# Optimization experiments

Measured on AMD Instinct MI355X. Metric: run time of the kernel, lower is better.

Reference implementation:

```python
import jax, jax.numpy as jnp
import numpy as np

LN_EPS = 1e-6
KERNEL_EPS = 1e-3  # fast_attention generalized kernel_epsilon


def layer_norm(x, scale, bias):
    mu = jnp.mean(x, axis=-1, keepdims=True)
    var = jnp.mean(jnp.square(x - mu), axis=-1, keepdims=True)
    return (x - mu) * jax.lax.rsqrt(var + LN_EPS) * scale + bias


def sinusoidal_pos_emb(seq_len, dim):
    pos = jnp.arange(seq_len, dtype=jnp.float32)[:, None]
    div = jnp.exp(jnp.arange(0, dim, 2, dtype=jnp.float32) * (-np.log(10000.0) / dim))
    pe = jnp.zeros((seq_len, dim), dtype=jnp.float32)
    pe = pe.at[:, 0::2].set(jnp.sin(pos * div)).at[:, 1::2].set(jnp.cos(pos * div))
    return pe


def favor_generalized_attention(x, mask, wq, wk, wv, wo):
    # x: [B,S,E], mask: [B,S,1] (1 for real tokens), wq/wk/wv: [E,H,D], wo: [H,D,E]
    q = jnp.einsum('bse,ehd->bshd', x, wq)
    k = jnp.einsum('bse,ehd->bshd', x, wk)
    v = jnp.einsum('bse,ehd->bshd', x, wv)
    # deterministic generalized features: phi(x) = relu(x) + eps
    phi_q = jax.nn.relu(q) + KERNEL_EPS
    phi_k = (jax.nn.relu(k) + KERNEL_EPS) * mask[..., None]  # zero padded keys
    # bidirectional linear attention: O(S * H * D^2)
    kv = jnp.einsum('bshm,bshd->bhmd', phi_k, v)      # [B,H,D,D]
    z = jnp.sum(phi_k, axis=1)                        # [B,H,D]
    num = jnp.einsum('bshm,bhmd->bshd', phi_q, kv)    # [B,S,H,D]
    den = jnp.einsum('bshm,bhm->bsh', phi_q, z)       # [B,S,H]
    out = num / den[..., None]
    return jnp.einsum('bshd,hde->bse', out, wo)


def setup_inputs() -> dict:
    key = jax.random.key(0)
    B, S, V, E, H, D, M, L = 4, 4096, 32000, 512, 8, 64, 2048, 6
    ks = jax.random.split(key, 8)
    w_scale = 0.02
    return {
        'inputs': jax.random.randint(ks[0], (B, S), 0, V, dtype=jnp.int32),
        'embed': jax.random.normal(ks[1], (V, E), jnp.float32),
        'ln1_scale': jnp.ones((L, E), jnp.float32),
        'ln1_bias': jnp.zeros((L, E), jnp.float32),
        'wq': jax.random.normal(ks[2], (L, E, H, D), jnp.float32) * w_scale,
        'wk': jax.random.normal(ks[3], (L, E, H, D), jnp.float32) * w_scale,
        'wv': jax.random.normal(ks[4], (L, E, H, D), jnp.float32) * w_scale,
        'wo': jax.random.normal(ks[5], (L, H, D, E), jnp.float32) * w_scale,
        'ln2_scale': jnp.ones((L, E), jnp.float32),
        'ln2_bias': jnp.zeros((L, E), jnp.float32),
        'w1': jax.random.normal(ks[6], (L, E, M), jnp.float32) * w_scale,
        'b1': jnp.zeros((L, M), jnp.float32),
        'w2': jax.random.normal(ks[7], (L, M, E), jnp.float32) * w_scale,
        'b2': jnp.zeros((L, E), jnp.float32),
        'lnf_scale': jnp.ones((E,), jnp.float32),
        'lnf_bias': jnp.zeros((E,), jnp.float32),
    }


def reference(inputs, embed, ln1_scale, ln1_bias, wq, wk, wv, wo,
              ln2_scale, ln2_bias, w1, b1, w2, b2, lnf_scale, lnf_bias):
    B, S = inputs.shape
    E = embed.shape[1]
    L = wq.shape[0]
    mask = (inputs > 0).astype(embed.dtype)[..., None]  # [B,S,1] padding mask
    x = embed[inputs]                                   # [B,S,E]
    x = x + sinusoidal_pos_emb(S, E)[None]
    for l in range(L):
        h = layer_norm(x, ln1_scale[l], ln1_bias[l])
        h = favor_generalized_attention(h, mask, wq[l], wk[l], wv[l], wo[l])
        x = x + h
        y = layer_norm(x, ln2_scale[l], ln2_bias[l])
        y = jax.nn.gelu(y @ w1[l] + b1[l]) @ w2[l] + b2[l]
        x = x + y
    return layer_norm(x, lnf_scale, lnf_bias)
```

## Files before the change

kernel.cpp:

```cpp
#include <hip/hip_runtime.h>
#include <hip/hip_bf16.h>

#define BATCH 4
#define SEQ   4096
#define BS_TOK (BATCH*SEQ)
#define EMB   512
#define NH    8
#define HD    64
#define FF    2048
#define NL    6

typedef unsigned short u16;
typedef __attribute__((ext_vector_type(8))) short bf16x8;
typedef __attribute__((ext_vector_type(4))) float f32x4;

__device__ __forceinline__ float bf2f(u16 u) {
    union { unsigned int i; float f; } x; x.i = ((unsigned int)u) << 16; return x.f;
}
__device__ __forceinline__ u16 f2bf(float f) {
    __hip_bfloat16 b = __float2bfloat16(f);
    return *(u16*)&b;
}
__device__ __forceinline__ float gelu_tanh(float x) {
    float x3 = x * x * x;
    return 0.5f * x * (1.f + tanhf(0.7978845608028654f * (x + 0.044715f * x3)));
}
__device__ __forceinline__ void store_out(float* p, float v) { *p = v; }
__device__ __forceinline__ void store_out(u16* p, float v) { *p = f2bf(v); }

__device__ __forceinline__ void gl_lds16(const void* g, void* l) {
    __builtin_amdgcn_global_load_lds(
        (__attribute__((address_space(1))) void*)g,
        (__attribute__((address_space(3))) void*)l, 16, 0, 0);
}

__global__ __launch_bounds__(128) void embed_kernel(
        const int* __restrict__ tok, const float* __restrict__ emb,
        float* __restrict__ X, float* __restrict__ maskf) {
    int row = blockIdx.x;
    int t = threadIdx.x;
    int id = tok[row];
    if (t == 0) maskf[row] = (id > 0) ? 1.f : 0.f;
    int s = row & (SEQ - 1);
    int e0 = t * 4;
    float4 u = *(const float4*)(emb + (size_t)id * EMB + e0);
    float vals[4] = { u.x, u.y, u.z, u.w };
    float out[4];
#pragma unroll
    for (int j = 0; j < 4; ++j) {
        int ee = e0 + j;
        int i = ee >> 1;
        float div = expf(-0.035977892078031970f * (float)i);
        float ang = (float)s * div;
        float pe = (ee & 1) ? cosf(ang) : sinf(ang);
        out[j] = vals[j] + pe;
    }
    *(float4*)(X + (size_t)row * EMB + e0) = make_float4(out[0], out[1], out[2], out[3]);
}

template<typename OUT>
__global__ __launch_bounds__(256) void ln_kernel(
        const float* __restrict__ X, const float* __restrict__ sc,
        const float* __restrict__ bi, OUT* __restrict__ Y) {
    int row = blockIdx.x, t = threadIdx.x;
    const float* x = X + (size_t)row * EMB;
    float a = x[t], b = x[t + 256];
    float s = a + b, q = a * a + b * b;
#pragma unroll
    for (int off = 32; off; off >>= 1) {
        s += __shfl_xor(s, off);
        q += __shfl_xor(q, off);
    }
    __shared__ float ss[4], qq[4];
    int w = t >> 6;
    if ((t & 63) == 0) { ss[w] = s; qq[w] = q; }
    __syncthreads();
    s = ss[0] + ss[1] + ss[2] + ss[3];
    q = qq[0] + qq[1] + qq[2] + qq[3];
    float mu = s * (1.f / 512.f);
    float var = q * (1.f / 512.f) - mu * mu;
    float rstd = rsqrtf(var + 1e-6f);
    float y0 = (a - mu) * rstd * sc[t] + bi[t];
    float y1 = (b - mu) * rstd * sc[t + 256] + bi[t + 256];
    store_out(&Y[(size_t)row * EMB + t], y0);
    store_out(&Y[(size_t)row * EMB + t + 256], y1);
}

__global__ __launch_bounds__(256) void transpose_w(
        const float* __restrict__ W0, const float* __restrict__ W1,
        const float* __restrict__ W2, const float* __restrict__ W3,
        u16* __restrict__ WT, int K, int N) {
    const float* W = (blockIdx.z == 0) ? W0 : (blockIdx.z == 1) ? W1
                   : (blockIdx.z == 2) ? W2 : W3;
    u16* dst = WT + (size_t)blockIdx.z * K * N;
    __shared__ u16 tile[32][33];
    int n0 = blockIdx.x * 32, k0 = blockIdx.y * 32;
    int tx = threadIdx.x & 31, ty = threadIdx.x >> 5;
#pragma unroll
    for (int u = 0; u < 4; ++u)
        tile[ty + u * 8][tx] = f2bf(W[(size_t)(k0 + ty + u * 8) * N + n0 + tx]);
    __syncthreads();
#pragma unroll
    for (int u = 0; u < 4; ++u)
        dst[(size_t)(n0 + ty + u * 8) * K + k0 + tx] = tile[tx][ty + u * 8];
}

template<int OP, typename OUT>
__global__ __launch_bounds__(256, 2) void mfma_gemm(
        const u16* __restrict__ A, const u16* __restrict__ BT,
        const float* __restrict__ bias, const float* __restrict__ rowscale,
        const float* __restrict__ residual, OUT* __restrict__ C,
        int K, int lda, int ldb, int ldc) {
    __shared__ u16 As[2 * 128 * 32];
    __shared__ u16 Bs[2 * 128 * 32];
    int tid = threadIdx.x;
    int wid = tid >> 6, lane = tid & 63;
    int row0 = blockIdx.y * 128, col0 = blockIdx.x * 128;
    int wm = (wid & 1) * 64, wn = (wid >> 1) * 64;
    int quad = lane >> 4, l16 = lane & 15;

    f32x4 acc[4][4];
#pragma unroll
    for (int i = 0; i < 4; ++i)
#pragma unroll
        for (int j = 0; j < 4; ++j)
#pragma unroll
            for (int r = 0; r < 4; ++r) acc[i][j][r] = 0.f;

    int rsub = lane >> 2;
    int koff = (lane & 3) * 8;
    const u16* gA = A  + (size_t)(row0 + wid * 16 + rsub) * lda + koff;
    const u16* gB = BT + (size_t)(col0 + wid * 16 + rsub) * ldb + koff;
    u16* lA = As + wid * 512;
    u16* lB = Bs + wid * 512;

    for (int k0 = 0; k0 < K; k0 += 64) {
#pragma unroll
        for (int p = 0; p < 2; ++p) {
#pragma unroll
            for (int i = 0; i < 2; ++i) {
                gl_lds16(gA + (size_t)(i * 64) * lda + p * 32, lA + p * 4096 + i * 2048);
                gl_lds16(gB + (size_t)(i * 64) * ldb + p * 32, lB + p * 4096 + i * 2048);
            }
        }
        gA += 64; gB += 64;
        __syncthreads();
#pragma unroll
        for (int h = 0; h < 2; ++h) {
            bf16x8 af[4], bfv[4];
#pragma unroll
            for (int i = 0; i < 4; ++i)
                af[i] = *(const bf16x8*)(As + h * 4096 + (wm + i * 16 + l16) * 32 + quad * 8);
#pragma unroll
            for (int j = 0; j < 4; ++j)
                bfv[j] = *(const bf16x8*)(Bs + h * 4096 + (wn + j * 16 + l16) * 32 + quad * 8);
#pragma unroll
            for (int i = 0; i < 4; ++i)
#pragma unroll
                for (int j = 0; j < 4; ++j)
                    acc[i][j] = __builtin_amdgcn_mfma_f32_16x16x32_bf16(af[i], bfv[j], acc[i][j], 0, 0, 0);
        }
        __syncthreads();
    }

    int seg = col0 >> 9;
    float bc[4];
#pragma unroll
    for (int j = 0; j < 4; ++j)
        bc[j] = bias ? bias[col0 + wn + j * 16 + l16] : 0.f;
#pragma unroll
    for (int i = 0; i < 4; ++i) {
        float res[4][4];
        if (residual) {
#pragma unroll
            for (int r = 0; r < 4; ++r) {
                size_t rb = (size_t)(row0 + wm + i * 16 + quad * 4 + r) * ldc + col0 + wn;
#pragma unroll
                for (int j = 0; j < 4; ++j)
                    res[r][j] = residual[rb + j * 16 + l16];
            }
        }
#pragma unroll
        for (int r = 0; r < 4; ++r) {
            int row = row0 + wm + i * 16 + quad * 4 + r;
            float rsv = (OP == 3 && seg == 1) ? rowscale[row] : 1.f;
            size_t rb = (size_t)row * ldc + col0 + wn;
#pragma unroll
            for (int j = 0; j < 4; ++j) {
                float val = acc[i][j][r] + bc[j];
                if (OP == 1) val = gelu_tanh(val);
                if (OP == 3 && seg < 2) val = fmaxf(val, 0.f) + 1e-3f;
                if (OP == 3 && seg == 1) val *= rsv;
                size_t idx = rb + j * 16 + l16;
                if (residual) val += res[r][j];
                store_out(&C[idx], val);
            }
        }
    }
}

__global__ __launch_bounds__(256) void kv_reduce_mfma(
        const u16* __restrict__ PK, const u16* __restrict__ V,
        float* __restrict__ KV, float* __restrict__ Z, int ld) {
    __shared__ __align__(16) u16 pks[32][68];
    __shared__ __align__(16) u16 vvs[32][68];
    int bh = blockIdx.x;
    int b = bh >> 3, hh = bh & 7;
    int cc = blockIdx.y;
    int t = threadIdx.x;
    int wid = t >> 6, lane = t & 63;
    int quad = lane >> 4, l16 = lane & 15;
    int wm = (wid & 1) * 32, wd = (wid >> 1) * 32;

    f32x4 acc[2][2];
    f32x4 zacc[2];
#pragma unroll
    for (int i = 0; i < 2; ++i) {
#pragma unroll
        for (int j = 0; j < 2; ++j)
#pragma unroll
            for (int r = 0; r < 4; ++r) acc[i][j][r] = 0.f;
#pragma unroll
        for (int r = 0; r < 4; ++r) zacc[i][r] = 0.f;
    }
    bf16x8 ones;
#pragma unroll
    for (int e = 0; e < 8; ++e) ones[e] = (short)0x3F80;

    int s_l = t >> 3, mo = (t & 7) * 8;
    const u16* gP = PK + (size_t)(b * SEQ + cc * 256 + s_l) * ld + hh * 64 + mo;
    const u16* gV = V  + (size_t)(b * SEQ + cc * 256 + s_l) * ld + hh * 64 + mo;
    ushort4 p0 = *(const ushort4*)gP;
    ushort4 p1 = *(const ushort4*)(gP + 4);
    ushort4 q0 = *(const ushort4*)gV;
    ushort4 q1 = *(const ushort4*)(gV + 4);

    for (int st = 0; st < 8; ++st) {
        *(ushort4*)&pks[s_l][mo]     = p0;
        *(ushort4*)&pks[s_l][mo + 4] = p1;
        *(ushort4*)&vvs[s_l][mo]     = q0;
        *(ushort4*)&vvs[s_l][mo + 4] = q1;
        __syncthreads();
        if (st < 7) {
            gP += (size_t)32 * ld;  gV += (size_t)32 * ld;
            p0 = *(const ushort4*)gP;  p1 = *(const ushort4*)(gP + 4);
            q0 = *(const ushort4*)gV;  q1 = *(const ushort4*)(gV + 4);
        }
        bf16x8 af[2], bfv[2];
#pragma unroll
        for (int i = 0; i < 2; ++i) {
#pragma unroll
            for (int e = 0; e < 8; ++e) {
                af[i][e]  = (short)pks[quad * 8 + e][wm + i * 16 + l16];
                bfv[i][e] = (short)vvs[quad * 8 + e][wd + i * 16 + l16];
            }
        }
#pragma unroll
        for (int i = 0; i < 2; ++i)
#pragma unroll
            for (int j = 0; j < 2; ++j)
                acc[i][j] = __builtin_amdgcn_mfma_f32_16x16x32_bf16(af[i], bfv[j], acc[i][j], 0, 0, 0);
        if (wid < 2) {
            zacc[0] = __builtin_amdgcn_mfma_f32_16x16x32_bf16(af[0], ones, zacc[0], 0, 0, 0);
            zacc[1] = __builtin_amdgcn_mfma_f32_16x16x32_bf16(af[1], ones, zacc[1], 0, 0, 0);
        }
        __syncthreads();
    }

#pragma unroll
    for (int i = 0; i < 2; ++i)
#pragma unroll
        for (int j = 0; j < 2; ++j)
#pragma unroll
            for (int r = 0; r < 4; ++r)
                atomicAdd(&KV[((size_t)bh * 64 + wm + i * 16 + quad * 4 + r) * 64
                              + wd + j * 16 + l16], acc[i][j][r]);
    if (wid < 2 && l16 == 0) {
#pragma unroll
        for (int i = 0; i < 2; ++i)
#pragma unroll
            for (int r = 0; r < 4; ++r)
                atomicAdd(&Z[(size_t)bh * 64 + wm + i * 16 + quad * 4 + r], zacc[i][r]);
    }
}

__global__ __launch_bounds__(256) void attn_out2(
        const u16* __restrict__ PQ, const float* __restrict__ KV,
        const float* __restrict__ Z, u16* __restrict__ O, int ld) {
    __shared__ float kvT[64 * 65];
    __shared__ float zsh[64];
    __shared__ float phs[4][72];
    int hh = blockIdx.y;
    int row0 = blockIdx.x * 32;
    int b = row0 >> 12;
    int bh = b * NH + hh;
    int t = threadIdx.x;
    const float* kvg = KV + (size_t)bh * 4096;
#pragma unroll
    for (int u = 0; u < 16; ++u) {
        int idx = u * 256 + t;
        kvT[(idx & 63) * 65 + (idx >> 6)] = kvg[idx];
    }
    if (t < 64) zsh[t] = Z[(size_t)bh * 64 + t];
    __syncthreads();
    int wid = t >> 6, lane = t & 63;
    const float* kvrow = kvT + lane * 65;
    for (int rr = 0; rr < 8; ++rr) {
        int row = row0 + wid * 8 + rr;
        float p = bf2f(PQ[(size_t)row * ld + hh * 64 + lane]);
        float d = p * zsh[lane];
#pragma unroll
        for (int off = 32; off; off >>= 1) d += __shfl_xor(d, off);
        d = fmaxf(d, 1e-20f);
        phs[wid][lane] = p;
        float acc = 0.f;
#pragma unroll
        for (int mm = 0; mm < 64; ++mm)
            acc = fmaf(phs[wid][mm], kvrow[mm], acc);
        O[(size_t)row * EMB + hh * 64 + lane] = f2bf(acc / d);
    }
}

extern "C" void kernel_launch(void* const* d_in, const int* in_sizes, int n_in,
                              void* d_out, int out_size, void* d_ws, size_t ws_size,
                              hipStream_t stream) {
    (void)in_sizes; (void)n_in; (void)out_size; (void)ws_size;
    const int*   tok  = (const int*)d_in[0];
    const float* emb  = (const float*)d_in[1];
    const float* ln1s = (const float*)d_in[2];
    const float* ln1b = (const float*)d_in[3];
    const float* wq   = (const float*)d_in[4];
    const float* wk   = (const float*)d_in[5];
    const float* wv   = (const float*)d_in[6];
    const float* wo   = (const float*)d_in[7];
    const float* ln2s = (const float*)d_in[8];
    const float* ln2b = (const float*)d_in[9];
    const float* w1   = (const float*)d_in[10];
    const float* b1   = (const float*)d_in[11];
    const float* w2   = (const float*)d_in[12];
    const float* b2   = (const float*)d_in[13];
    const float* lnfs = (const float*)d_in[14];
    const float* lnfb = (const float*)d_in[15];

    char* ws = (char*)d_ws;
    const size_t MB = 1024 * 1024;
    float* x    = (float*)(ws);
    u16*   h    = (u16*)(ws + 32 * MB);
    u16*   qkv  = (u16*)(ws + 48 * MB);
    u16*   m    = qkv;
    float* kv   = (float*)(ws + 96 * MB);
    float* z    = kv + BATCH * NH * HD * HD;
    float* maskf = (float*)(ws + 96 * MB + 768 * 1024);
    u16*   wt   = (u16*)(ws + 97 * MB);
    u16*   w1t  = (u16*)(ws + 99 * MB);
    u16*   w2t  = (u16*)(ws + 101 * MB);

    embed_kernel<<<BS_TOK, 128, 0, stream>>>(tok, emb, x, maskf);

    const size_t WSTEP = (size_t)EMB * EMB;
    dim3 gQKV(12, BS_TOK / 128);
    dim3 gN512(4, BS_TOK / 128);
    dim3 gN1024(8, BS_TOK / 128);

    for (int l = 0; l < NL; ++l) {
        ln_kernel<u16><<<BS_TOK, 256, 0, stream>>>(x, ln1s + l * EMB, ln1b + l * EMB, h);
        transpose_w<<<dim3(16, 16, 4), 256, 0, stream>>>(
            wq + l * WSTEP, wk + l * WSTEP, wv + l * WSTEP, wo + l * WSTEP, wt, EMB, EMB);
        mfma_gemm<3, u16><<<gQKV, 256, 0, stream>>>(
            h, wt, nullptr, maskf, nullptr, qkv, EMB, EMB, EMB, 1536);

        hipMemsetAsync(kv, 0, (size_t)(BATCH * NH * HD * HD + BATCH * NH * HD) * sizeof(float), stream);
        kv_reduce_mfma<<<dim3(BATCH * NH, SEQ / 256), 256, 0, stream>>>(qkv + 512, qkv + 1024, kv, z, 1536);
        attn_out2<<<dim3(BS_TOK / 32, NH), 256, 0, stream>>>(qkv, kv, z, h, 1536);

        mfma_gemm<0, float><<<gN512, 256, 0, stream>>>(
            h, wt + 3 * WSTEP, nullptr, nullptr, x, x, EMB, EMB, EMB, EMB);

        ln_kernel<u16><<<BS_TOK, 256, 0, stream>>>(x, ln2s + l * EMB, ln2b + l * EMB, h);
        const float* w1l = w1 + (size_t)l * EMB * FF;
        const float* w2l = w2 + (size_t)l * FF * EMB;
        const float* b1l = b1 + (size_t)l * FF;
        const float* b2l = b2 + (size_t)l * EMB;
        transpose_w<<<dim3(64, 16, 1), 256, 0, stream>>>(w1l, w1l, w1l, w1l, w1t, EMB, FF);
        transpose_w<<<dim3(16, 64, 1), 256, 0, stream>>>(w2l, w2l, w2l, w2l, w2t, FF, EMB);
        for (int c = 0; c < 2; ++c) {
            mfma_gemm<1, u16><<<gN1024, 256, 0, stream>>>(
                h, w1t + (size_t)c * 1024 * EMB, b1l + c * 1024, nullptr, nullptr, m,
                EMB, EMB, EMB, 1024);
            mfma_gemm<0, float><<<gN512, 256, 0, stream>>>(
                m, w2t + (size_t)c * 1024, (c == 0 ? b2l : nullptr), nullptr, x, x,
                1024, 1024, FF, EMB);
        }
    }

    ln_kernel<float><<<BS_TOK, 256, 0, stream>>>(x, lnfs, lnfb, (float*)d_out);
}
```

Before: 1.857 ms.

## Double-buffer GEMM LDS tiles with K=32 prefetch and swizzle workgroup order

Restructures the GEMM main loop from a load-all-then-compute step over K=64 into a ping-pong double buffer over K=32 slices. The next slice's global-to-LDS load is issued before the current slice's MFMAs, so memory latency can overlap compute, and one barrier per iteration is dropped. It also remaps workgroup IDs in groups of 8 to change which tiles run concurrently, aiming for better L2 reuse. The trade-off is half as much MFMA work between barriers, and correctness relies on each async LDS load being complete when the barrier is reached.

Result: no change. 1.843 ms (-0.8%).

```diff
diff --git a/kernel.cpp b/kernel.cpp
--- a/kernel.cpp
+++ b/kernel.cpp
@@ -111,11 +111,15 @@
         const float* __restrict__ bias, const float* __restrict__ rowscale,
         const float* __restrict__ residual, OUT* __restrict__ C,
         int K, int lda, int ldb, int ldc) {
-    __shared__ u16 As[2 * 128 * 32];
-    __shared__ u16 Bs[2 * 128 * 32];
+    __shared__ u16 As[2][128 * 32];
+    __shared__ u16 Bs[2][128 * 32];
     int tid = threadIdx.x;
     int wid = tid >> 6, lane = tid & 63;
-    int row0 = blockIdx.y * 128, col0 = blockIdx.x * 128;
+    int nwg = gridDim.x * gridDim.y;
+    int lin = blockIdx.y * gridDim.x + blockIdx.x;
+    int swz = (nwg & 7) ? lin : ((lin & 7) * (nwg >> 3) + (lin >> 3));
+    int bx = swz % gridDim.x, by = swz / gridDim.x;
+    int row0 = by * 128, col0 = bx * 128;
     int wm = (wid & 1) * 64, wn = (wid >> 1) * 64;
     int quad = lane >> 4, l16 = lane & 15;
 
@@ -131,35 +135,35 @@
     int koff = (lane & 3) * 8;
     const u16* gA = A  + (size_t)(row0 + wid * 16 + rsub) * lda + koff;
     const u16* gB = BT + (size_t)(col0 + wid * 16 + rsub) * ldb + koff;
-    u16* lA = As + wid * 512;
-    u16* lB = Bs + wid * 512;
-
-    for (int k0 = 0; k0 < K; k0 += 64) {
-#pragma unroll
-        for (int p = 0; p < 2; ++p) {
-#pragma unroll
-            for (int i = 0; i < 2; ++i) {
-                gl_lds16(gA + (size_t)(i * 64) * lda + p * 32, lA + p * 4096 + i * 2048);
-                gl_lds16(gB + (size_t)(i * 64) * ldb + p * 32, lB + p * 4096 + i * 2048);
-            }
-        }
-        gA += 64; gB += 64;
-        __syncthreads();
-#pragma unroll
-        for (int h = 0; h < 2; ++h) {
-            bf16x8 af[4], bfv[4];
-#pragma unroll
-            for (int i = 0; i < 4; ++i)
-                af[i] = *(const bf16x8*)(As + h * 4096 + (wm + i * 16 + l16) * 32 + quad * 8);
+
+    auto stage = [&](int bb, int kk) {
+        u16* lA = As[bb] + wid * 512;
+        u16* lB = Bs[bb] + wid * 512;
+#pragma unroll
+        for (int i = 0; i < 2; ++i) {
+            gl_lds16(gA + (size_t)(i * 64) * lda + kk, lA + i * 2048);
+            gl_lds16(gB + (size_t)(i * 64) * ldb + kk, lB + i * 2048);
+        }
+    };
+
+    int nt = K >> 5;
+    stage(0, 0);
+    __syncthreads();
+    for (int t = 0; t < nt; ++t) {
+        int cur = t & 1;
+        if (t + 1 < nt) stage(cur ^ 1, (t + 1) * 32);
+        bf16x8 af[4], bfv[4];
+#pragma unroll
+        for (int i = 0; i < 4; ++i)
+            af[i] = *(const bf16x8*)(As[cur] + (wm + i * 16 + l16) * 32 + quad * 8);
+#pragma unroll
+        for (int j = 0; j < 4; ++j)
+            bfv[j] = *(const bf16x8*)(Bs[cur] + (wn + j * 16 + l16) * 32 + quad * 8);
+#pragma unroll
+        for (int i = 0; i < 4; ++i)
 #pragma unroll
             for (int j = 0; j < 4; ++j)
-                bfv[j] = *(const bf16x8*)(Bs + h * 4096 + (wn + j * 16 + l16) * 32 + quad * 8);
-#pragma unroll
-            for (int i = 0; i < 4; ++i)
-#pragma unroll
-                for (int j = 0; j < 4; ++j)
-                    acc[i][j] = __builtin_amdgcn_mfma_f32_16x16x32_bf16(af[i], bfv[j], acc[i][j], 0, 0, 0);
-        }
+                acc[i][j] = __builtin_amdgcn_mfma_f32_16x16x32_bf16(af[i], bfv[j], acc[i][j], 0, 0, 0);
         __syncthreads();
     }
 
```
